# Optimization experiments

Hardware: AMD Instinct MI355X
Metric: run time of the kernel (lower is better)

## Reference

```python
import jax, jax.numpy as jnp
import numpy as np

EMBED_DIM = 512
BLOCK = 511
N_HEAD = 8
N_GLOBAL = 4
N_LOCAL = 2
N_MIX = 2
RECEP = 4
T = 2 * BLOCK + 2  # [task, clip, BLOCK upper, BLOCK lower]
HD = EMBED_DIM // N_HEAD
NEG = -1e9


def _build_masks():
    bs = BLOCK
    temporal = np.concatenate([np.zeros(2), np.arange(bs) * 2 + 1, np.arange(bs) * 2 + 2])
    seq = temporal[None, :] <= temporal[:, None]  # causal over interleaved temporal order
    tq = np.concatenate([np.arange(bs) * 2 + 1 - 2 * RECEP + 1] * 2)
    tk = np.concatenate([np.arange(bs) * 2 + 1] * 2)
    de = tk[None, :] < tq[:, None]  # keys too far in the past for the sliding window
    local = seq.copy()
    local[2:, 2:] = local[2:, 2:] & ~de
    return jnp.asarray(local), jnp.asarray(seq)


LOCAL_MASK, GLOBAL_MASK = _build_masks()  # (T, T) bool, True = visible


def _linear_params(key, fan_in, fan_out):
    k1, k2 = jax.random.split(key)
    s = 1.0 / np.sqrt(fan_in)
    W = jax.random.uniform(k1, (fan_out, fan_in), minval=-s, maxval=s, dtype=jnp.float32)
    b = jax.random.uniform(k2, (fan_out,), minval=-s, maxval=s, dtype=jnp.float32)
    return W, b


def setup_inputs() -> dict:
    key = jax.random.key(0)
    ks = jax.random.split(key, 10)
    B = 4
    x = jax.random.normal(ks[0], (B, T, EMBED_DIM), dtype=jnp.float32)
    cond_mask = jnp.ones((B, T), dtype=jnp.float32)
    Wq, bq = _linear_params(ks[1], EMBED_DIM, EMBED_DIM)
    Wk, bk = _linear_params(ks[2], EMBED_DIM, EMBED_DIM)
    Wv, bv = _linear_params(ks[3], EMBED_DIM, EMBED_DIM)
    Wqml, bqml = _linear_params(ks[4], EMBED_DIM, HD * N_MIX)
    Wkml, bkml = _linear_params(ks[5], EMBED_DIM, HD * N_MIX)
    Wp, bp = _linear_params(ks[6], EMBED_DIM, EMBED_DIM)
    mix_w = jax.random.normal(ks[7], (N_MIX, 2), dtype=jnp.float32) * 0.5  # Conv2d(2*nm, nm, groups=nm, 1x1)
    bias_clip = jnp.full((1, N_HEAD, 1), 0.5, dtype=jnp.float32)
    bias_clip_ml = jnp.full((1, N_MIX, 1), 0.5, dtype=jnp.float32)
    return dict(x=x, cond_mask=cond_mask, Wq=Wq, bq=bq, Wk=Wk, bk=bk, Wv=Wv, bv=bv,
                Wqml=Wqml, bqml=bqml, Wkml=Wkml, bkml=bkml, mix_w=mix_w, Wp=Wp, bp=bp,
                bias_clip=bias_clip, bias_clip_ml=bias_clip_ml)


def reference(x, cond_mask, Wq, bq, Wk, bk, Wv, bv, Wqml, bqml, Wkml, bkml, mix_w, Wp, bp, bias_clip, bias_clip_ml):
    B, Tx, C = x.shape

    def heads(W, b, nh):
        return (x @ W.T + b).reshape(B, Tx, nh, HD).transpose(0, 2, 1, 3)  # (B, nh, T, hd)

    q = heads(Wq, bq, N_HEAD)
    k = heads(Wk, bk, N_HEAD)
    v = heads(Wv, bv, N_HEAD)
    qml = heads(Wqml, bqml, N_MIX)
    kml = heads(Wkml, bkml, N_MIX)

    scale = 1.0 / np.sqrt(HD)
    # main attention: heads [0:N_LOCAL] local-masked, rest global (causal) masked
    att = jnp.einsum('bhqd,bhkd->bhqk', q, k) * scale
    att = att.at[:, :, :, 1].add(bias_clip)  # learned bias on the CLIP-token key column
    head_mask = jnp.concatenate([
        jnp.broadcast_to(LOCAL_MASK, (N_LOCAL, Tx, Tx)),
        jnp.broadcast_to(GLOBAL_MASK, (N_MIX + N_GLOBAL, Tx, Tx))], axis=0)
    att = jax.nn.softmax(jnp.where(head_mask[None], att, NEG), axis=-1)

    # extra local-masked score maps for the mix heads
    aml = jnp.einsum('bhqd,bhkd->bhqk', qml, kml) * scale
    aml = aml.at[:, :, :, 1].add(bias_clip_ml)
    aml = jax.nn.softmax(jnp.where(LOCAL_MASK[None, None], aml, NEG), axis=-1)

    # grouped 1x1 conv: per mix head, blend (global, local) attention maps
    mix_in = jnp.stack([att[:, N_LOCAL:N_LOCAL + N_MIX], aml], axis=2)  # (B, nm, 2, T, T)
    mix_out = jnp.einsum('ho,bhoqk->bhqk', mix_w, mix_in)

    att_f = jnp.concatenate([att[:, :N_LOCAL], mix_out, att[:, N_LOCAL + N_MIX:]], axis=1)
    y = jnp.einsum('bhqk,bhkd->bhqd', att_f, v)
    y = y.transpose(0, 2, 1, 3).reshape(B, Tx, C)
    return y @ Wp.T + bp
```

## Files before the change

kernel.cpp:

```cpp
#include <hip/hip_runtime.h>

typedef unsigned short u16;
typedef __attribute__((ext_vector_type(8))) __bf16 bf16x8;
typedef __attribute__((ext_vector_type(4))) float f32x4;
typedef __attribute__((ext_vector_type(8))) short short8;
typedef __attribute__((ext_vector_type(4))) u16 us4;
typedef __attribute__((ext_vector_type(4))) unsigned u32x4;

#define T_SEQ 1024
#define PW 1280
#define QSC 0.18033688f
#define L2E 1.4426950408889634f

__device__ __forceinline__ u16 f2bf(float f) {
  unsigned u = __float_as_uint(f);
  u += 0x7fff + ((u >> 16) & 1);
  return (u16)(u >> 16);
}
__device__ __forceinline__ float bf2f(u16 v) {
  return __uint_as_float((unsigned)v << 16);
}

__constant__ u16 GLOB_M[16] = {0x0101,0x0303,0x0707,0x0F0F,0x1F1F,0x3F3F,0x7F7F,0xFFFF,
                               0xFFFF,0x0307,0x070F,0x0F1F,0x1F3F,0x3F7F,0x7FFF,0xFFFF};
__constant__ u16 LOC_M[16]  = {0x0101,0x0303,0x0607,0x0C0D,0x1819,0x3031,0x6061,0xC0C1,
                               0x8183,0x0307,0x060F,0x0C1D,0x1839,0x3071,0x60E1,0xC1C1};

__device__ __forceinline__ void gll16(const u16* gp, u16* lp) {
  __builtin_amdgcn_global_load_lds((const __attribute__((address_space(1))) unsigned*)gp,
                                   (__attribute__((address_space(3))) unsigned*)lp, 16, 0, 0);
}

template<int NISS>
__device__ __forceinline__ void stage_sw(u16* lds, const u16* __restrict__ g,
                                         int ld, int tid) {
  const int w = tid >> 6;
#pragma unroll
  for (int i = 0; i < NISS; ++i) {
    int row = i * 32 + (tid >> 3);
    int cswz = ((tid & 7) << 4) ^ ((row & 7) << 4);
    gll16(g + (size_t)row * ld + (cswz >> 1), lds + i * 2048 + w * 512);
  }
}

__device__ __forceinline__ void stage8(u16* lds, const u16* __restrict__ g,
                                       int ld, int tid) {
  int row = tid >> 3;
  int cswz = (((tid & 7) << 4) ^ ((row & 7) << 4)) >> 1;
  gll16(g + (size_t)row * ld + cswz, lds + (tid >> 6) * 512);
}

__device__ __forceinline__ bf16x8 rd_sw(const u16* lds, int row, int colbyte) {
  return *(const bf16x8*)&lds[row * 64 + ((colbyte ^ ((row & 7) << 4)) >> 1)];
}

__global__ void prep_all(const float4* __restrict__ x, u16* __restrict__ xb,
                         const float* __restrict__ Wq, const float* __restrict__ Wk,
                         const float* __restrict__ Wv, const float* __restrict__ Wqml,
                         const float* __restrict__ Wkml, const float* __restrict__ Wp,
                         const float* __restrict__ bq, const float* __restrict__ bk,
                         const float* __restrict__ bv, const float* __restrict__ bqml,
                         const float* __restrict__ bkml,
                         u16* __restrict__ Wcat, u16* __restrict__ Wpx, float* __restrict__ bcat) {
  if (blockIdx.x < 2048) {
    int i = blockIdx.x * 256 + threadIdx.x;
    float4 v = x[i];
    us4 o = { f2bf(v.x), f2bf(v.y), f2bf(v.z), f2bf(v.w) };
    *(us4*)&xb[i * 4] = o;
    return;
  }
  int idx = (blockIdx.x - 2048) * 256 + threadIdx.x;
  const int NW = 1792 * 512;
  if (idx < NW) {
    int row = idx >> 9;
    float v;
    if (row < 512)       v = Wq[idx];
    else if (row < 1024) v = Wk[idx - 512 * 512];
    else if (row < 1536) v = Wv[idx - 1024 * 512];
    else if (row < 1664) v = Wqml[idx - 1536 * 512];
    else                 v = Wkml[idx - 1664 * 512];
    Wcat[idx] = f2bf(v);
    return;
  }
  int i2 = idx - NW;
  if (i2 < 512 * 640) {
    int n = i2 / 640, k2 = i2 - n * 640;
    float v = (k2 < 512) ? Wp[n * 512 + k2] : Wp[n * 512 + k2 - 384];
    Wpx[i2] = f2bf(v);
    return;
  }
  int i3 = i2 - 512 * 640;
  if (i3 < 1792) {
    float v;
    if (i3 < 512)       v = bq[i3];
    else if (i3 < 1024) v = bk[i3 - 512];
    else if (i3 < 1536) v = bv[i3 - 1024];
    else if (i3 < 1664) v = bqml[i3 - 1536];
    else                v = bkml[i3 - 1664];
    bcat[i3] = v;
  }
}

__global__ __launch_bounds__(256) void gemm_qkv(
    const u16* __restrict__ A, const u16* __restrict__ Bw,
    const float* __restrict__ bias, u16* __restrict__ Pout, u16* __restrict__ Vtb) {
  __shared__ u16 As[2][8192];
  __shared__ u16 Bs[2][8192];
  const int tid = threadIdx.x;
  const int lane = tid & 63, w = tid >> 6;
  const int g = lane >> 4, c = lane & 15;
  const int n0 = blockIdx.x * 128, m0 = blockIdx.y * 128;
  const int wm = (w >> 1) * 64, wn = (w & 1) * 64;

  f32x4 acc[4][4] = {};
  stage_sw<4>(As[0], A + (size_t)m0 * 512, 512, tid);
  stage_sw<4>(Bs[0], Bw + (size_t)n0 * 512, 512, tid);
  __syncthreads();
  for (int ks = 0; ks < 8; ++ks) {
    int cur = ks & 1;
    if (ks + 1 < 8) {
      stage_sw<4>(As[cur ^ 1], A + (size_t)m0 * 512 + (ks + 1) * 64, 512, tid);
      stage_sw<4>(Bs[cur ^ 1], Bw + (size_t)n0 * 512 + (ks + 1) * 64, 512, tid);
    }
#pragma unroll
    for (int h = 0; h < 2; ++h) {
      bf16x8 av[4], bv[4];
#pragma unroll
      for (int f = 0; f < 4; ++f) {
        av[f] = rd_sw(As[cur], wm + f * 16 + c, h * 64 + g * 16);
        bv[f] = rd_sw(Bs[cur], wn + f * 16 + c, h * 64 + g * 16);
      }
#pragma unroll
      for (int fm = 0; fm < 4; ++fm)
#pragma unroll
        for (int fn = 0; fn < 4; ++fn)
          acc[fm][fn] = __builtin_amdgcn_mfma_f32_16x16x32_bf16(av[fm], bv[fn], acc[fm][fn], 0, 0, 0);
    }
    __syncthreads();
  }

  const bool isV = (n0 >= 1024 && n0 < 1536);
#pragma unroll
  for (int fm = 0; fm < 4; ++fm)
#pragma unroll
    for (int fn = 0; fn < 4; ++fn) {
      int row = m0 + wm + fm * 16 + g * 4;
      int col = n0 + wn + fn * 16 + c;
      float bb = bias[col];
      if (isV) {
        int d = col - 1024;
        int bidx = row >> 10, t = row & 1023;
        us4 pack = { f2bf(acc[fm][fn][0] + bb), f2bf(acc[fm][fn][1] + bb),
                     f2bf(acc[fm][fn][2] + bb), f2bf(acc[fm][fn][3] + bb) };
        *(us4*)&Vtb[((size_t)bidx * 512 + d) * 1024 + t] = pack;
      } else {
        float sc = (col < 512 || (col >= 1536 && col < 1664)) ? QSC : 1.0f;
        int pcol = (col < 1024) ? col : col - 512;
#pragma unroll
        for (int r = 0; r < 4; ++r)
          Pout[(size_t)(row + r) * PW + pcol] = f2bf((acc[fm][fn][r] + bb) * sc);
      }
    }
}

__global__ __launch_bounds__(256) void gemm_out(
    const u16* __restrict__ A, const u16* __restrict__ Bw,
    const float* __restrict__ bias, float* __restrict__ Cout) {
  __shared__ u16 As[2][8192];
  __shared__ u16 Bs[2][4096];
  const int tid = threadIdx.x;
  const int lane = tid & 63, w = tid >> 6;
  const int g = lane >> 4, c = lane & 15;
  const int n0 = blockIdx.x * 64, m0 = blockIdx.y * 128;
  const int wm = (w >> 1) * 64, wn = (w & 1) * 32;

  f32x4 acc[4][2] = {};
  stage_sw<4>(As[0], A + (size_t)m0 * 640, 640, tid);
  stage_sw<2>(Bs[0], Bw + (size_t)n0 * 640, 640, tid);
  __syncthreads();
  for (int ks = 0; ks < 10; ++ks) {
    int cur = ks & 1;
    if (ks + 1 < 10) {
      stage_sw<4>(As[cur ^ 1], A + (size_t)m0 * 640 + (ks + 1) * 64, 640, tid);
      stage_sw<2>(Bs[cur ^ 1], Bw + (size_t)n0 * 640 + (ks + 1) * 64, 640, tid);
    }
#pragma unroll
    for (int h = 0; h < 2; ++h) {
      bf16x8 av[4], bv[2];
#pragma unroll
      for (int f = 0; f < 4; ++f)
        av[f] = rd_sw(As[cur], wm + f * 16 + c, h * 64 + g * 16);
#pragma unroll
      for (int f = 0; f < 2; ++f)
        bv[f] = rd_sw(Bs[cur], wn + f * 16 + c, h * 64 + g * 16);
#pragma unroll
      for (int fm = 0; fm < 4; ++fm)
#pragma unroll
        for (int fn = 0; fn < 2; ++fn)
          acc[fm][fn] = __builtin_amdgcn_mfma_f32_16x16x32_bf16(av[fm], bv[fn], acc[fm][fn], 0, 0, 0);
    }
    __syncthreads();
  }
#pragma unroll
  for (int fm = 0; fm < 4; ++fm)
#pragma unroll
    for (int fn = 0; fn < 2; ++fn)
#pragma unroll
      for (int r = 0; r < 4; ++r) {
        int row = m0 + wm + fm * 16 + g * 4 + r;
        int col = n0 + wn + fn * 16 + c;
        Cout[(size_t)row * 512 + col] = acc[fm][fn][r] + bias[col];
      }
}

__global__ __launch_bounds__(512, 8) void attn_k(
    const u16* __restrict__ P, const u16* __restrict__ Vtb,
    u16* __restrict__ Part_o, float* __restrict__ Part_ml,
    const float* __restrict__ bias_clip, const float* __restrict__ bias_clip_ml) {
  __shared__ u16 Ks[2][4096];
  __shared__ u16 Vs[2][4096];
  const int tid = threadIdx.x, lane = tid & 63, w = tid >> 6;
  const int g = lane >> 4, c = lane & 15;
  const int qt2 = blockIdx.x, u = blockIdx.y, b = blockIdx.z;

  int qcol, kcol, vsel;
  bool localMask;
  float kbias;
  unsigned mask;
  unsigned uni = (unsigned)LOC_M[2 * qt2] | (unsigned)LOC_M[2 * qt2 + 1];
  if (u < 24) {
    int h = 2 + (u >> 2), sp = u & 3;
    qcol = h * 64; kcol = 512 + h * 64; vsel = h; kbias = bias_clip[h];
    localMask = false;
    mask = ((unsigned)GLOB_M[2 * qt2] | (unsigned)GLOB_M[2 * qt2 + 1]) & (0x1111u << sp);
  } else if (u < 28) {
    int h = (u - 24) >> 1, sp = (u - 24) & 1;
    qcol = h * 64; kcol = 512 + h * 64; vsel = h; kbias = bias_clip[h];
    localMask = true;
    mask = uni & (sp ? 0xAAAAu : 0x5555u);
  } else {
    int mh = (u - 28) >> 1, sp = (u - 28) & 1;
    qcol = 1024 + mh * 64; kcol = 1152 + mh * 64; vsel = 2 + mh; kbias = bias_clip_ml[mh];
    localMask = true;
    mask = uni & (sp ? 0xAAAAu : 0x5555u);
  }
  kbias *= L2E;
  const size_t baseP = (size_t)b * T_SEQ * PW;
  const u16* __restrict__ Kbase = P + baseP + kcol;
  const u16* __restrict__ Vbase = Vtb + ((size_t)b * 512 + vsel * 64) * 1024;
  const int r0 = qt2 * 128 + w * 16;
  const int qg = r0 + c;

  int tq = (qg < 2) ? 0 : ((qg < 513) ? 2 * qg - 3 : 2 * qg - 1024);
  int upmax = (tq - 1) >> 1;
  int lomax = (tq - 2) >> 1;
  int wmin = (localMask && qg >= 2) ? ((qg < 513 ? qg - 2 : qg - 513) - 3) : -1000000;

  float mM = -1e8f, lL = 0.0f;
  f32x4 o[4] = {};

  if (mask) {
    bf16x8 aq0 = *(const bf16x8*)&P[baseP + (size_t)qg * PW + qcol + g * 8];
    bf16x8 aq1 = *(const bf16x8*)&P[baseP + (size_t)qg * PW + qcol + 32 + g * 8];

    unsigned rem = mask;
    int kt_cur = __ffs(rem) - 1; rem &= rem - 1;
    stage8(Ks[0], Kbase + (size_t)(kt_cur * 64) * PW, PW, tid);
    stage8(Vs[0], Vbase + kt_cur * 64, 1024, tid);
    int kt_nxt = -1;
    if (rem) {
      kt_nxt = __ffs(rem) - 1; rem &= rem - 1;
      stage8(Ks[1], Kbase + (size_t)(kt_nxt * 64) * PW, PW, tid);
      stage8(Vs[1], Vbase + kt_nxt * 64, 1024, tid);
    }
    int cur = 0;

    for (;;) {
      if (kt_nxt >= 0) asm volatile("s_waitcnt vmcnt(2)" ::: "memory");
      else             asm volatile("s_waitcnt vmcnt(0)" ::: "memory");
      __builtin_amdgcn_sched_barrier(0);
      __builtin_amdgcn_s_barrier();

      const int k0 = kt_cur * 64;

      float s[4][4];
#pragma unroll
      for (int cb = 0; cb < 4; ++cb) {
        f32x4 accs = {};
        bf16x8 bk0 = rd_sw(Ks[cur], cb * 16 + c, g * 16);
        bf16x8 bk1 = rd_sw(Ks[cur], cb * 16 + c, 64 + g * 16);
        accs = __builtin_amdgcn_mfma_f32_16x16x32_bf16(bk0, aq0, accs, 0, 0, 0);
        accs = __builtin_amdgcn_mfma_f32_16x16x32_bf16(bk1, aq1, accs, 0, 0, 0);
#pragma unroll
        for (int r = 0; r < 4; ++r) s[cb][r] = accs[r];
      }

#pragma unroll
      for (int cb = 0; cb < 4; ++cb) {
        int kb = k0 + cb * 16 + g * 4;
#pragma unroll
        for (int r = 0; r < 4; ++r) {
          int kk = kb + r;
          bool tok = kk < 2;
          bool low = kk >= 513;
          int jk = kk - (low ? 513 : 2);
          int bnd = low ? lomax : upmax;
          bool vis = tok | ((jk <= bnd) & (jk >= wmin));
          float addb = (kk == 1) ? kbias : 0.0f;
          s[cb][r] = vis ? (s[cb][r] + addb) : -1e9f;
        }
      }

      float rmax = s[0][0];
#pragma unroll
      for (int cb = 0; cb < 4; ++cb)
#pragma unroll
        for (int r = 0; r < 4; ++r) rmax = fmaxf(rmax, s[cb][r]);
      rmax = fmaxf(rmax, __shfl_xor(rmax, 16));
      rmax = fmaxf(rmax, __shfl_xor(rmax, 32));
      float mnew = fmaxf(mM, rmax);
      float fr = exp2f(mM - mnew);
      float psum = 0.0f;
#pragma unroll
      for (int cb = 0; cb < 4; ++cb)
#pragma unroll
        for (int r = 0; r < 4; ++r) {
          float p = exp2f(s[cb][r] - mnew);
          s[cb][r] = p;
          psum += p;
        }
      psum += __shfl_xor(psum, 16);
      psum += __shfl_xor(psum, 32);
      lL = lL * fr + psum;
      mM = mnew;
#pragma unroll
      for (int db = 0; db < 4; ++db) o[db] *= fr;

      unsigned wpk[4][2];
#pragma unroll
      for (int cb = 0; cb < 4; ++cb) {
        asm("v_cvt_pk_bf16_f32 %0, %1, %2" : "=v"(wpk[cb][0]) : "v"(s[cb][0]), "v"(s[cb][1]));
        asm("v_cvt_pk_bf16_f32 %0, %1, %2" : "=v"(wpk[cb][1]) : "v"(s[cb][2]), "v"(s[cb][3]));
      }
#pragma unroll
      for (int ks2 = 0; ks2 < 2; ++ks2) {
        unsigned tw[4];
#pragma unroll
        for (int rr = 0; rr < 2; ++rr) {
          unsigned L = wpk[2 * ks2][rr], H = wpk[2 * ks2 + 1][rr];
          unsigned sA = (g & 1) ? L : H;
          unsigned sB = (g & 1) ? H : L;
          unsigned X16 = (unsigned)__shfl_xor((int)sA, 16);
          unsigned X32 = (unsigned)__shfl_xor((int)sA, 32);
          unsigned X48 = (unsigned)__shfl_xor((int)sB, 48);
          unsigned a  = (g >= 2) ? ((g == 3) ? X16 : X32) : ((g == 1) ? X48 : L);
          unsigned b2 = (g >= 2) ? ((g == 3) ? H : X48) : ((g == 1) ? X32 : X16);
          tw[rr] = a; tw[2 + rr] = b2;
        }
        u32x4 tw4 = { tw[0], tw[1], tw[2], tw[3] };
        bf16x8 ap = __builtin_bit_cast(bf16x8, tw4);
#pragma unroll
        for (int db = 0; db < 4; ++db) {
          bf16x8 av = rd_sw(Vs[cur], db * 16 + c, ks2 * 64 + g * 16);
          o[db] = __builtin_amdgcn_mfma_f32_16x16x32_bf16(av, ap, o[db], 0, 0, 0);
        }
      }

      __builtin_amdgcn_s_barrier();
      if (kt_nxt < 0) break;
      int kt_nn = -1;
      if (rem) {
        kt_nn = __ffs(rem) - 1; rem &= rem - 1;
        stage8(Ks[cur], Kbase + (size_t)(kt_nn * 64) * PW, PW, tid);
        stage8(Vs[cur], Vbase + kt_nn * 64, 1024, tid);
      }
      kt_cur = kt_nxt; kt_nxt = kt_nn; cur ^= 1;
    }
  }

  u16* po = Part_o + ((size_t)(u * 4 + b)) * T_SEQ * 64;
#pragma unroll
  for (int db = 0; db < 4; ++db) {
    us4 pk = { f2bf(o[db][0]), f2bf(o[db][1]), f2bf(o[db][2]), f2bf(o[db][3]) };
    *(us4*)&po[(size_t)qg * 64 + db * 16 + g * 4] = pk;
  }
  if (g == 0) {
    float2 ml = { mM, lL };
    *(float2*)&Part_ml[(((size_t)(u * 4 + b)) * T_SEQ + qg) * 2] = ml;
  }
}

__global__ __launch_bounds__(256) void combine_k(
    const u16* __restrict__ Part_o, const float* __restrict__ Part_ml,
    u16* __restrict__ Y, const float* __restrict__ mix_w) {
  int idx = blockIdx.x * 256 + threadIdx.x;
  int q4 = idx & 15;
  int row = (idx >> 4) & 1023;
  int bb = (idx >> 14) & 3;
  int j = idx >> 16;
  int ns, bs, outcol;
  float wgt;
  if (j < 6)      { ns = 4; bs = j * 4;            outcol = 128 + j * 64;       wgt = (j < 2) ? mix_w[2 * j] : 1.0f; }
  else if (j < 8) { ns = 2; bs = 24 + (j - 6) * 2; outcol = (j - 6) * 64;       wgt = 1.0f; }
  else            { ns = 2; bs = 28 + (j - 8) * 2; outcol = 512 + (j - 8) * 64; wgt = mix_w[(j - 8) * 2 + 1]; }

  float mv[4], lv[4];
  float ms = -1e30f;
  for (int s = 0; s < ns; ++s) {
    size_t base = (((size_t)(bs + s) * 4 + bb) * 1024 + row) * 2;
    mv[s] = Part_ml[base];
    lv[s] = Part_ml[base + 1];
    ms = fmaxf(ms, mv[s]);
  }
  float denom = 0.0f, e[4];
  for (int s = 0; s < ns; ++s) { e[s] = exp2f(mv[s] - ms); denom += lv[s] * e[s]; }
  float inv = wgt / denom;
  float out[4] = {0.f, 0.f, 0.f, 0.f};
  for (int s = 0; s < ns; ++s) {
    us4 ov = *(const us4*)&Part_o[(((size_t)(bs + s) * 4 + bb) * 1024 + row) * 64 + q4 * 4];
#pragma unroll
    for (int t = 0; t < 4; ++t) out[t] += e[s] * bf2f(ov[t]);
  }
  us4 pk = { f2bf(out[0] * inv), f2bf(out[1] * inv), f2bf(out[2] * inv), f2bf(out[3] * inv) };
  *(us4*)&Y[((size_t)bb * 1024 + row) * 640 + outcol + q4 * 4] = pk;
}

extern "C" void kernel_launch(void* const* d_in, const int* in_sizes, int n_in,
                              void* d_out, int out_size, void* d_ws, size_t ws_size,
                              hipStream_t stream) {
  const float* x     = (const float*)d_in[0];
  const float* Wq    = (const float*)d_in[2];
  const float* bq    = (const float*)d_in[3];
  const float* Wk    = (const float*)d_in[4];
  const float* bk    = (const float*)d_in[5];
  const float* Wv    = (const float*)d_in[6];
  const float* bv    = (const float*)d_in[7];
  const float* Wqml  = (const float*)d_in[8];
  const float* bqml  = (const float*)d_in[9];
  const float* Wkml  = (const float*)d_in[10];
  const float* bkml  = (const float*)d_in[11];
  const float* mixw  = (const float*)d_in[12];
  const float* Wp    = (const float*)d_in[13];
  const float* bp    = (const float*)d_in[14];
  const float* bclip = (const float*)d_in[15];
  const float* bclipml = (const float*)d_in[16];

  u16* xb   = (u16*)d_ws;
  u16* Wcat = xb + 4096 * 512;
  u16* Wpx  = Wcat + 1792 * 512;
  u16* Ybuf = Wpx + 512 * 640;
  u16* Vtb  = Ybuf + 4096 * 640;
  u16* Pbuf = Vtb + 4 * 512 * 1024;
  float* bcat = (float*)(Pbuf + 4096 * 1280);
  u16* Part_o = (u16*)(bcat + 2048);
  float* Part_ml = (float*)(Part_o + 32 * 4 * 1024 * 64);

  prep_all<<<6919, 256, 0, stream>>>((const float4*)x, xb, Wq, Wk, Wv, Wqml, Wkml, Wp,
                                     bq, bk, bv, bqml, bkml, Wcat, Wpx, bcat);
  gemm_qkv<<<dim3(14, 32), 256, 0, stream>>>(xb, Wcat, bcat, Pbuf, Vtb);
  attn_k<<<dim3(8, 32, 4), 512, 0, stream>>>(Pbuf, Vtb, Part_o, Part_ml, bclip, bclipml);
  combine_k<<<2560, 256, 0, stream>>>(Part_o, Part_ml, Ybuf, mixw);
  gemm_out<<<dim3(8, 32), 256, 0, stream>>>(Ybuf, Wpx, bp, (float*)d_out);
}
```

Before: 83.97 us.

## Stage all key/value tiles up front instead of double-buffered pipeline

Each attention block now loads every K/V tile it needs (at most four, from the split mask) into four shared-memory slots at once. It then does one wait and one barrier and runs all tiles with no further synchronisation. This removes the per-iteration barriers and the rolling double-buffer bookkeeping. In exchange, shared memory per block doubles, the launch-bounds occupancy hint drops from 8 to 4, and compute no longer overlaps later loads.

```diff
diff --git a/kernel.cpp b/kernel.cpp
--- a/kernel.cpp
+++ b/kernel.cpp
@@ -213,12 +213,12 @@
       }
 }
 
-__global__ __launch_bounds__(512, 8) void attn_k(
+__global__ __launch_bounds__(512, 4) void attn_k(
     const u16* __restrict__ P, const u16* __restrict__ Vtb,
     u16* __restrict__ Part_o, float* __restrict__ Part_ml,
     const float* __restrict__ bias_clip, const float* __restrict__ bias_clip_ml) {
-  __shared__ u16 Ks[2][4096];
-  __shared__ u16 Vs[2][4096];
+  __shared__ u16 Ks[4][4096];
+  __shared__ u16 Vs[4][4096];
   const int tid = threadIdx.x, lane = tid & 63, w = tid >> 6;
   const int g = lane >> 4, c = lane & 15;
   const int qt2 = blockIdx.x, u = blockIdx.y, b = blockIdx.z;
@@ -263,32 +263,33 @@
     bf16x8 aq0 = *(const bf16x8*)&P[baseP + (size_t)qg * PW + qcol + g * 8];
     bf16x8 aq1 = *(const bf16x8*)&P[baseP + (size_t)qg * PW + qcol + 32 + g * 8];
 
+    const int nt = __popc(mask);
+    int kts[4] = {0, 0, 0, 0};
     unsigned rem = mask;
-    int kt_cur = __ffs(rem) - 1; rem &= rem - 1;
-    stage8(Ks[0], Kbase + (size_t)(kt_cur * 64) * PW, PW, tid);
-    stage8(Vs[0], Vbase + kt_cur * 64, 1024, tid);
-    int kt_nxt = -1;
-    if (rem) {
-      kt_nxt = __ffs(rem) - 1; rem &= rem - 1;
-      stage8(Ks[1], Kbase + (size_t)(kt_nxt * 64) * PW, PW, tid);
-      stage8(Vs[1], Vbase + kt_nxt * 64, 1024, tid);
-    }
-    int cur = 0;
-
-    for (;;) {
-      if (kt_nxt >= 0) asm volatile("s_waitcnt vmcnt(2)" ::: "memory");
-      else             asm volatile("s_waitcnt vmcnt(0)" ::: "memory");
-      __builtin_amdgcn_sched_barrier(0);
-      __builtin_amdgcn_s_barrier();
-
-      const int k0 = kt_cur * 64;
+#pragma unroll
+    for (int j = 0; j < 4; ++j) {
+      if (j < nt) {
+        int kt = __ffs(rem) - 1; rem &= rem - 1;
+        kts[j] = kt;
+        stage8(Ks[j], Kbase + (size_t)(kt * 64) * PW, PW, tid);
+        stage8(Vs[j], Vbase + kt * 64, 1024, tid);
+      }
+    }
+    asm volatile("s_waitcnt vmcnt(0)" ::: "memory");
+    __builtin_amdgcn_sched_barrier(0);
+    __builtin_amdgcn_s_barrier();
+
+#pragma unroll
+    for (int j = 0; j < 4; ++j) {
+      if (j >= nt) break;
+      const int k0 = kts[j] * 64;
 
       float s[4][4];
 #pragma unroll
       for (int cb = 0; cb < 4; ++cb) {
         f32x4 accs = {};
-        bf16x8 bk0 = rd_sw(Ks[cur], cb * 16 + c, g * 16);
-        bf16x8 bk1 = rd_sw(Ks[cur], cb * 16 + c, 64 + g * 16);
+        bf16x8 bk0 = rd_sw(Ks[j], cb * 16 + c, g * 16);
+        bf16x8 bk1 = rd_sw(Ks[j], cb * 16 + c, 64 + g * 16);
         accs = __builtin_amdgcn_mfma_f32_16x16x32_bf16(bk0, aq0, accs, 0, 0, 0);
         accs = __builtin_amdgcn_mfma_f32_16x16x32_bf16(bk1, aq1, accs, 0, 0, 0);
 #pragma unroll
@@ -361,20 +362,10 @@
         bf16x8 ap = __builtin_bit_cast(bf16x8, tw4);
 #pragma unroll
         for (int db = 0; db < 4; ++db) {
-          bf16x8 av = rd_sw(Vs[cur], db * 16 + c, ks2 * 64 + g * 16);
+          bf16x8 av = rd_sw(Vs[j], db * 16 + c, ks2 * 64 + g * 16);
           o[db] = __builtin_amdgcn_mfma_f32_16x16x32_bf16(av, ap, o[db], 0, 0, 0);
         }
       }
-
-      __builtin_amdgcn_s_barrier();
-      if (kt_nxt < 0) break;
-      int kt_nn = -1;
-      if (rem) {
-        kt_nn = __ffs(rem) - 1; rem &= rem - 1;
-        stage8(Ks[cur], Kbase + (size_t)(kt_nn * 64) * PW, PW, tid);
-        stage8(Vs[cur], Vbase + kt_nn * 64, 1024, tid);
-      }
-      kt_cur = kt_nxt; kt_nxt = kt_nn; cur ^= 1;
     }
   }
 
```

Measured after the change: 76.97 us. 1.09x faster.
